# Performance work log

Measured on AMD Instinct MI355X. Metric: run time of the kernel, lower is better.

The kernel has to match this reference:

```python
import jax, jax.numpy as jnp
import numpy as np

B, S, DEC, ENC, ATTN = 64, 1024, 1024, 1024, 1024

def setup_inputs() -> dict:
    key = jax.random.key(0)
    k1, k2, k3, k4, k5 = jax.random.split(key, 5)
    hidden = jax.random.normal(k1, (B, DEC), dtype=jnp.float32)
    encoder_outputs = jax.random.normal(k2, (B, S, ENC), dtype=jnp.float32)
    # nn.Linear(dec+enc -> attn_dim): weight [attn, dec+enc], bias [attn]
    fan_in = DEC + ENC
    bound = 1.0 / np.sqrt(fan_in)
    W_attn = jax.random.uniform(k3, (ATTN, fan_in), dtype=jnp.float32, minval=-bound, maxval=bound)
    b_attn = jax.random.uniform(k4, (ATTN,), dtype=jnp.float32, minval=-bound, maxval=bound)
    # v = torch.rand(attn_dim) -> uniform [0,1)
    v = jax.random.uniform(k5, (ATTN,), dtype=jnp.float32)
    return {"hidden": hidden, "encoder_outputs": encoder_outputs,
            "W_attn": W_attn, "b_attn": b_attn, "v": v}

def reference(hidden, encoder_outputs, W_attn, b_attn, v):
    # hidden: [B, DEC], encoder_outputs: [B, S, ENC]
    b, s, _ = encoder_outputs.shape
    h = jnp.broadcast_to(hidden[:, None, :], (b, s, hidden.shape[-1]))
    combined = jnp.concatenate([h, encoder_outputs], axis=-1)        # [B, S, DEC+ENC]
    energy = jnp.tanh(jnp.einsum('bsf,af->bsa', combined, W_attn) + b_attn)  # [B, S, ATTN]
    scores = jnp.einsum('bsa,a->bs', energy, v)                      # [B, S]
    attn_weights = jax.nn.softmax(scores, axis=1)                    # [B, S]
    context = jnp.einsum('bs,bse->be', attn_weights, encoder_outputs)[:, None, :]  # [B, 1, ENC]
    return context
```

## Files before the change

kernel.cpp:

```cpp
#include <hip/hip_runtime.h>
#include <hip/hip_bf16.h>
#include <stdint.h>

#define NB 64
#define NS 1024
#define NE 1024
#define NA 1024
#define NF 2048
#define LDP 144

typedef __attribute__((ext_vector_type(8))) short   short8;
typedef __attribute__((ext_vector_type(4))) short   short4v;
typedef __attribute__((ext_vector_type(4))) float   f32x4;
typedef __attribute__((ext_vector_type(8))) __bf16  bf16x8;

__device__ __forceinline__ unsigned short f2bf(float x) {
  union { float f; unsigned u; } v; v.f = x;
  unsigned r = v.u + 0x7fffu + ((v.u >> 16) & 1u);
  return (unsigned short)(r >> 16);
}
__device__ __forceinline__ float bf2f(unsigned short h) {
  union { unsigned u; float f; } v; v.u = ((unsigned)h) << 16;
  return v.f;
}
__device__ __forceinline__ float tanh_fast(float x) {
  float e = __expf(2.0f * x);
  return 1.0f - __fdividef(2.0f, e + 1.0f);
}
__device__ __forceinline__ short8 pack8(float4 a, float4 b) {
  short8 h;
  h[0]=(short)f2bf(a.x); h[1]=(short)f2bf(a.y); h[2]=(short)f2bf(a.z); h[3]=(short)f2bf(a.w);
  h[4]=(short)f2bf(b.x); h[5]=(short)f2bf(b.y); h[6]=(short)f2bf(b.z); h[7]=(short)f2bf(b.w);
  return h;
}
__device__ __forceinline__ void gload_lds16(const void* g, void* l) {
  __builtin_amdgcn_global_load_lds((const __attribute__((address_space(1))) void*)g,
                                   (__attribute__((address_space(3))) void*)l, 16, 0, 0);
}

__global__ __launch_bounds__(256) void k_pre(const float* __restrict__ hidden,
                                             const float* __restrict__ W,
                                             const float* __restrict__ bias,
                                             float* __restrict__ u_,
                                             float4* __restrict__ scz,
                                             float4* __restrict__ outz,
                                             short8* __restrict__ Wb,
                                             const float4* __restrict__ encf,
                                             short8* __restrict__ encb) {
  const int bid = blockIdx.x;
  const int tid = threadIdx.x;
  if (bid < 512) {
    const int l = tid & 63;
    const int w = tid >> 6;
    const int a = (bid >> 1) * 4 + w;
    const int bh = bid & 1;
    const float* wrow = W + (size_t)a * NF;
    float4 wv[4];
    #pragma unroll
    for (int i = 0; i < 4; ++i) wv[i] = *(const float4*)(wrow + l * 4 + i * 256);
    const float ba = bias[a];
    for (int b = bh * 32; b < bh * 32 + 32; ++b) {
      const float* hrow = hidden + b * 1024;
      float s = 0.f;
      #pragma unroll
      for (int i = 0; i < 4; ++i) {
        float4 hv = *(const float4*)(hrow + l * 4 + i * 256);
        s += wv[i].x * hv.x + wv[i].y * hv.y + wv[i].z * hv.z + wv[i].w * hv.w;
      }
      #pragma unroll
      for (int m = 1; m < 64; m <<= 1) s += __shfl_xor(s, m);
      if (l == 0) u_[b * NA + a] = s + ba;
    }
  } else if (bid < 640) {
    const int i = (bid - 512) * 256 + tid;
    float4 z; z.x = z.y = z.z = z.w = 0.f;
    if (i < 16384) scz[i] = z;
    else           outz[i - 16384] = z;
  } else if (bid < 1152) {
    const int id = (bid - 640) * 256 + tid;
    const int a = id >> 7, ku = id & 127;
    const float* s = W + (size_t)a * NF + 1024 + ku * 8;
    Wb[id] = pack8(*(const float4*)s, *(const float4*)(s + 4));
  } else {
    const int n8 = NB * NS * NE / 8;
    int i = (bid - 1152) * 256 + tid;
    const int stride = 2048 * 256;
    for (; i < n8; i += stride) {
      float4 a = encf[2 * i], b = encf[2 * i + 1];
      encb[i] = pack8(a, b);
    }
  }
}

__global__ __launch_bounds__(256) void k_zero(float4* __restrict__ p, int n4) {
  int i = blockIdx.x * 256 + threadIdx.x;
  if (i < n4) { float4 z; z.x = z.y = z.z = z.w = 0.f; p[i] = z; }
}
__global__ __launch_bounds__(256) void k_conv_w(const float* __restrict__ W, short8* __restrict__ dst) {
  const int id = blockIdx.x * 256 + threadIdx.x;
  const int a = id >> 7, ku = id & 127;
  const float* s = W + (size_t)a * NF + 1024 + ku * 8;
  dst[id] = pack8(*(const float4*)s, *(const float4*)(s + 4));
}
__global__ __launch_bounds__(256) void k_u(const float* __restrict__ hidden,
                                           const float* __restrict__ W,
                                           const float* __restrict__ bias,
                                           float* __restrict__ u) {
  const int l = threadIdx.x & 63;
  const int w = threadIdx.x >> 6;
  const int a = (blockIdx.x >> 1) * 4 + w;
  const int bh = blockIdx.x & 1;
  const float* wrow = W + (size_t)a * NF;
  float4 wv[4];
  #pragma unroll
  for (int i = 0; i < 4; ++i) wv[i] = *(const float4*)(wrow + l * 4 + i * 256);
  const float ba = bias[a];
  for (int b = bh * 32; b < bh * 32 + 32; ++b) {
    const float* hrow = hidden + b * 1024;
    float s = 0.f;
    #pragma unroll
    for (int i = 0; i < 4; ++i) {
      float4 hv = *(const float4*)(hrow + l * 4 + i * 256);
      s += wv[i].x * hv.x + wv[i].y * hv.y + wv[i].z * hv.z + wv[i].w * hv.w;
    }
    #pragma unroll
    for (int m = 1; m < 64; m <<= 1) s += __shfl_xor(s, m);
    if (l == 0) u[b * NA + a] = s + ba;
  }
}

__global__ __launch_bounds__(512, 2) void k_main256(const unsigned short* __restrict__ Ab,
                                                    const unsigned short* __restrict__ Bb,
                                                    const float* __restrict__ u_,
                                                    const float* __restrict__ v_,
                                                    float* __restrict__ scores) {
  __shared__ __align__(16) char smem[2 * 65536];

  const int tid = threadIdx.x;
  const int l = tid & 63;
  const int w = tid >> 6;
  const int wr = w >> 2, wc = w & 3;
  const int d = blockIdx.x;
  const int xcd = d & 7, q = d >> 3;
  const int rt = xcd * 32 + (q >> 2);
  const int ct = q & 3;
  const int b = rt >> 2;
  const int lh = l >> 4, l15 = l & 15, l7 = l & 7;

  const int ssk = ((tid & 7) ^ ((tid >> 3) & 7)) * 8;
  const unsigned short* aS = Ab + (size_t)(rt * 256 + (tid >> 3)) * NE + ssk;
  const unsigned short* bS = Bb + (size_t)(ct * 256 + (tid >> 3)) * NE + ssk;
  const int wdst = w * 1024;

  f32x4 acc[8][4] = {};

#define STAGE256(tt) do { \
    char* dst_ = smem + (((tt) & 1) << 16); \
    const unsigned short* a_ = aS + (size_t)(tt) * 64; \
    const unsigned short* b_ = bS + (size_t)(tt) * 64; \
    gload_lds16(a_,                    dst_ + wdst); \
    gload_lds16(a_ + (size_t) 64 * NE, dst_ +  64 * 128 + wdst); \
    gload_lds16(a_ + (size_t)128 * NE, dst_ + 128 * 128 + wdst); \
    gload_lds16(a_ + (size_t)192 * NE, dst_ + 192 * 128 + wdst); \
    gload_lds16(b_,                    dst_ + 32768 + wdst); \
    gload_lds16(b_ + (size_t) 64 * NE, dst_ + 32768 +  64 * 128 + wdst); \
    gload_lds16(b_ + (size_t)128 * NE, dst_ + 32768 + 128 * 128 + wdst); \
    gload_lds16(b_ + (size_t)192 * NE, dst_ + 32768 + 192 * 128 + wdst); } while (0)

  STAGE256(0);

  for (int t = 0; t < 16; ++t) {
    asm volatile("s_waitcnt vmcnt(0)" ::: "memory");
    asm volatile("s_barrier" ::: "memory");
    if (t < 15) STAGE256(t + 1);

    const char* As = smem + ((t & 1) << 16);
    const char* Bs = As + 32768;

    bf16x8 areg[8][2];
    #pragma unroll
    for (int rf = 0; rf < 8; ++rf)
      #pragma unroll
      for (int kh = 0; kh < 2; ++kh)
        areg[rf][kh] = *(const bf16x8*)(As + (wr * 128 + rf * 16 + l15) * 128
                                           + (((kh * 4 + lh) ^ l7) << 4));
    #pragma unroll
    for (int cfh = 0; cfh < 2; ++cfh) {
      bf16x8 breg[2][2];
      #pragma unroll
      for (int c2 = 0; c2 < 2; ++c2)
        #pragma unroll
        for (int kh = 0; kh < 2; ++kh)
          breg[c2][kh] = *(const bf16x8*)(Bs + (wc * 64 + (cfh * 2 + c2) * 16 + l15) * 128
                                             + (((kh * 4 + lh) ^ l7) << 4));
      __builtin_amdgcn_s_setprio(1);
      #pragma unroll
      for (int rf = 0; rf < 8; ++rf)
        #pragma unroll
        for (int c2 = 0; c2 < 2; ++c2)
          #pragma unroll
          for (int kh = 0; kh < 2; ++kh)
            acc[rf][cfh * 2 + c2] = __builtin_amdgcn_mfma_f32_16x16x32_bf16(
                areg[rf][kh], breg[c2][kh], acc[rf][cfh * 2 + c2], 0, 0, 0);
      __builtin_amdgcn_s_setprio(0);
    }
  }
#undef STAGE256

  const int colb = ct * 256 + wc * 64 + l15;
  float uv[4], vv[4];
  #pragma unroll
  for (int cf = 0; cf < 4; ++cf) {
    const int c = colb + cf * 16;
    uv[cf] = u_[b * NA + c];
    vv[cf] = v_[c];
  }
  #pragma unroll
  for (int rf = 0; rf < 8; ++rf) {
    #pragma unroll
    for (int reg = 0; reg < 4; ++reg) {
      float sacc = 0.f;
      #pragma unroll
      for (int cf = 0; cf < 4; ++cf)
        sacc += tanh_fast(acc[rf][cf][reg] + uv[cf]) * vv[cf];
      sacc += __shfl_xor(sacc, 1);
      sacc += __shfl_xor(sacc, 2);
      sacc += __shfl_xor(sacc, 4);
      sacc += __shfl_xor(sacc, 8);
      if (l15 == 0) {
        const int m = rt * 256 + wr * 128 + rf * 16 + lh * 4 + reg;
        atomicAdd(&scores[m], sacc);
      }
    }
  }
}

__global__ __launch_bounds__(256) void k_smctx(const float* __restrict__ sc,
                                               const unsigned short* __restrict__ encb,
                                               float* __restrict__ out) {
  const int b = blockIdx.x >> 4, scn = blockIdx.x & 15;
  const int t = threadIdx.x;
  __shared__ float rmax[4], rsum[4];
  __shared__ float wbuf[NS];

  float4 x = *(const float4*)(sc + b * NS + t * 4);
  float mx = fmaxf(fmaxf(x.x, x.y), fmaxf(x.z, x.w));
  #pragma unroll
  for (int m = 1; m < 64; m <<= 1) mx = fmaxf(mx, __shfl_xor(mx, m));
  if ((t & 63) == 0) rmax[t >> 6] = mx;
  __syncthreads();
  mx = fmaxf(fmaxf(rmax[0], rmax[1]), fmaxf(rmax[2], rmax[3]));
  float e0 = __expf(x.x - mx), e1 = __expf(x.y - mx);
  float e2 = __expf(x.z - mx), e3 = __expf(x.w - mx);
  float sm = e0 + e1 + e2 + e3;
  #pragma unroll
  for (int m = 1; m < 64; m <<= 1) sm += __shfl_xor(sm, m);
  if ((t & 63) == 0) rsum[t >> 6] = sm;
  __syncthreads();
  sm = rsum[0] + rsum[1] + rsum[2] + rsum[3];
  const float inv = 1.0f / sm;
  wbuf[t * 4 + 0] = e0 * inv;
  wbuf[t * 4 + 1] = e1 * inv;
  wbuf[t * 4 + 2] = e2 * inv;
  wbuf[t * 4 + 3] = e3 * inv;
  __syncthreads();

  float a0 = 0.f, a1 = 0.f, a2 = 0.f, a3 = 0.f;
  for (int s = scn * 64; s < scn * 64 + 64; ++s) {
    const float wv = wbuf[s];
    const size_t base = ((size_t)(b * NS + s)) * NE + t * 4;
    short4v hv = *(const short4v*)(encb + base);
    a0 += wv * bf2f((unsigned short)hv[0]);
    a1 += wv * bf2f((unsigned short)hv[1]);
    a2 += wv * bf2f((unsigned short)hv[2]);
    a3 += wv * bf2f((unsigned short)hv[3]);
  }
  float* c = out + b * NE + t * 4;
  atomicAdd(c + 0, a0); atomicAdd(c + 1, a1);
  atomicAdd(c + 2, a2); atomicAdd(c + 3, a3);
}

template <int ACONV, int BCONV>
__global__ __launch_bounds__(256) void k_main_rs(const void* __restrict__ Asrc,
                                                 const void* __restrict__ Bsrc,
                                                 const float* __restrict__ u_,
                                                 const float* __restrict__ v_,
                                                 float* __restrict__ scores) {
  __shared__ __align__(16) char smemf[2 * 128 * LDP];
  char* As = smemf;
  char* Bs = smemf + 128 * LDP;
  const int tid = threadIdx.x;
  const int l = tid & 63;
  const int w = tid >> 6;
  const int wr = w >> 1, wc = w & 1;
  const int d = blockIdx.x;
  const int rt = (d & 7) * 64 + (d >> 6);
  const int ct = (d >> 3) & 7;
  const int b = rt >> 3;
  const int l7 = l & 7, lh = l >> 4, l15 = l & 15;
  const int srow = w * 8 + (l >> 3);
  f32x4 acc[4][4] = {};
  for (int kt = 0; kt < 16; ++kt) {
    const int k0 = kt * 64;
    __syncthreads();
    #pragma unroll
    for (int r = 0; r < 4; ++r) {
      const int row = r * 32 + srow;
      short8 val;
      if constexpr (ACONV) {
        const float* s = (const float*)Asrc + (size_t)(rt * 128 + row) * NE + k0 + l7 * 8;
        val = pack8(*(const float4*)s, *(const float4*)(s + 4));
      } else {
        val = *(const short8*)((const unsigned short*)Asrc + (size_t)(rt * 128 + row) * NE + k0 + l7 * 8);
      }
      *(short8*)(As + row * LDP + l7 * 16) = val;
    }
    #pragma unroll
    for (int r = 0; r < 4; ++r) {
      const int row = r * 32 + srow;
      short8 val;
      if constexpr (BCONV) {
        const float* s = (const float*)Bsrc + (size_t)(ct * 128 + row) * NF + 1024 + k0 + l7 * 8;
        val = pack8(*(const float4*)s, *(const float4*)(s + 4));
      } else {
        val = *(const short8*)((const unsigned short*)Bsrc + (size_t)(ct * 128 + row) * NE + k0 + l7 * 8);
      }
      *(short8*)(Bs + row * LDP + l7 * 16) = val;
    }
    __syncthreads();
    #pragma unroll
    for (int ks = 0; ks < 2; ++ks) {
      bf16x8 af[4], bfr[4];
      const int ku = (ks * 4 + lh) * 16;
      #pragma unroll
      for (int f = 0; f < 4; ++f) {
        af[f]  = *(const bf16x8*)(As + (wr * 64 + f * 16 + l15) * LDP + ku);
        bfr[f] = *(const bf16x8*)(Bs + (wc * 64 + f * 16 + l15) * LDP + ku);
      }
      #pragma unroll
      for (int i = 0; i < 4; ++i)
        #pragma unroll
        for (int jj = 0; jj < 4; ++jj)
          acc[i][jj] = __builtin_amdgcn_mfma_f32_16x16x32_bf16(af[i], bfr[jj], acc[i][jj], 0, 0, 0);
    }
  }
  const int colb = ct * 128 + wc * 64 + l15;
  float uv[4], vv[4];
  #pragma unroll
  for (int jj = 0; jj < 4; ++jj) {
    const int c = colb + jj * 16;
    uv[jj] = u_[b * NA + c];
    vv[jj] = v_[c];
  }
  #pragma unroll
  for (int i = 0; i < 4; ++i) {
    #pragma unroll
    for (int reg = 0; reg < 4; ++reg) {
      float sacc = 0.f;
      #pragma unroll
      for (int jj = 0; jj < 4; ++jj)
        sacc += tanh_fast(acc[i][jj][reg] + uv[jj]) * vv[jj];
      sacc += __shfl_xor(sacc, 1);
      sacc += __shfl_xor(sacc, 2);
      sacc += __shfl_xor(sacc, 4);
      sacc += __shfl_xor(sacc, 8);
      if (l15 == 0) {
        const int m = rt * 128 + wr * 64 + i * 16 + lh * 4 + reg;
        atomicAdd(&scores[m], sacc);
      }
    }
  }
}

__global__ __launch_bounds__(256) void k_softmax(float* __restrict__ sc) {
  const int b = blockIdx.x, t = threadIdx.x;
  float4 x = *(float4*)(sc + b * NS + t * 4);
  float mx = fmaxf(fmaxf(x.x, x.y), fmaxf(x.z, x.w));
  #pragma unroll
  for (int m = 1; m < 64; m <<= 1) mx = fmaxf(mx, __shfl_xor(mx, m));
  __shared__ float rmax[4], rsum[4];
  if ((t & 63) == 0) rmax[t >> 6] = mx;
  __syncthreads();
  mx = fmaxf(fmaxf(rmax[0], rmax[1]), fmaxf(rmax[2], rmax[3]));
  float e0 = __expf(x.x - mx), e1 = __expf(x.y - mx);
  float e2 = __expf(x.z - mx), e3 = __expf(x.w - mx);
  float sm = e0 + e1 + e2 + e3;
  #pragma unroll
  for (int m = 1; m < 64; m <<= 1) sm += __shfl_xor(sm, m);
  if ((t & 63) == 0) rsum[t >> 6] = sm;
  __syncthreads();
  sm = rsum[0] + rsum[1] + rsum[2] + rsum[3];
  const float inv = 1.0f / sm;
  float4 o; o.x = e0 * inv; o.y = e1 * inv; o.z = e2 * inv; o.w = e3 * inv;
  *(float4*)(sc + b * NS + t * 4) = o;
}
template <int CONV>
__global__ __launch_bounds__(256) void k_ctx(const void* __restrict__ encsrc,
                                             const float* __restrict__ wgt,
                                             float* __restrict__ ctx) {
  const int b = blockIdx.x >> 4, scn = blockIdx.x & 15;
  const int t = threadIdx.x;
  float a0 = 0.f, a1 = 0.f, a2 = 0.f, a3 = 0.f;
  for (int s = scn * 64; s < scn * 64 + 64; ++s) {
    const float wv = wgt[b * NS + s];
    const size_t base = ((size_t)(b * NS + s)) * NE + t * 4;
    if constexpr (CONV) {
      float4 x = *((const float4*)((const float*)encsrc + base));
      a0 += wv * x.x; a1 += wv * x.y; a2 += wv * x.z; a3 += wv * x.w;
    } else {
      short4v hv = *(const short4v*)((const unsigned short*)encsrc + base);
      a0 += wv * bf2f((unsigned short)hv[0]);
      a1 += wv * bf2f((unsigned short)hv[1]);
      a2 += wv * bf2f((unsigned short)hv[2]);
      a3 += wv * bf2f((unsigned short)hv[3]);
    }
  }
  float* c = ctx + b * NE + t * 4;
  atomicAdd(c + 0, a0); atomicAdd(c + 1, a1);
  atomicAdd(c + 2, a2); atomicAdd(c + 3, a3);
}
__global__ __launch_bounds__(256) void k_out(const float* __restrict__ ctx,
                                             float* __restrict__ out) {
  const int i = blockIdx.x * 256 + threadIdx.x;
  float4 x = *(const float4*)(ctx + i * 4);
  *(float4*)(out + i * 4) = x;
}

extern "C" void kernel_launch(void* const* d_in, const int* in_sizes, int n_in,
                              void* d_out, int out_size, void* d_ws, size_t ws_size,
                              hipStream_t stream) {
  const float* hidden = (const float*)d_in[0];
  const float* enc    = (const float*)d_in[1];
  const float* W      = (const float*)d_in[2];
  const float* bias   = (const float*)d_in[3];
  const float* v      = (const float*)d_in[4];
  (void)in_sizes; (void)n_in; (void)out_size;

  char* ws = (char*)d_ws;
  const size_t T0 = (4ull << 20) + (128ull << 20);
  const size_t T1 = (3ull << 20);
  const int tier = (ws_size >= T0) ? 0 : ((ws_size >= T1) ? 1 : 2);

  unsigned short* Wb   = (unsigned short*)ws;
  unsigned short* encb = (unsigned short*)(ws + (4ull << 20));
  float* u_  = (tier < 2) ? (float*)(ws + (2ull << 20)) : (float*)ws;
  float* sc  = u_ + NB * NA;
  float* ctx = sc + NB * NS;

  if (tier == 0) {
    k_pre<<<3200, 256, 0, stream>>>(hidden, W, bias, u_, (float4*)sc, (float4*)d_out,
                                    (short8*)Wb, (const float4*)enc, (short8*)encb);
    k_main256<<<1024, 512, 0, stream>>>(encb, Wb, u_, v, sc);
    k_smctx<<<1024, 256, 0, stream>>>(sc, encb, (float*)d_out);
  } else if (tier == 1) {
    k_u<<<512, 256, 0, stream>>>(hidden, W, bias, u_);
    k_zero<<<128, 256, 0, stream>>>((float4*)sc, (NB * NS + NB * NE) / 4);
    k_conv_w<<<512, 256, 0, stream>>>(W, (short8*)Wb);
    k_main_rs<1, 0><<<4096, 256, 0, stream>>>(enc, Wb, u_, v, sc);
    k_softmax<<<64, 256, 0, stream>>>(sc);
    k_ctx<1><<<1024, 256, 0, stream>>>(enc, sc, ctx);
    k_out<<<64, 256, 0, stream>>>(ctx, (float*)d_out);
  } else {
    k_u<<<512, 256, 0, stream>>>(hidden, W, bias, u_);
    k_zero<<<128, 256, 0, stream>>>((float4*)sc, (NB * NS + NB * NE) / 4);
    k_main_rs<1, 1><<<4096, 256, 0, stream>>>(enc, W, u_, v, sc);
    k_softmax<<<64, 256, 0, stream>>>(sc);
    k_ctx<1><<<1024, 256, 0, stream>>>(enc, sc, ctx);
    k_out<<<64, 256, 0, stream>>>(ctx, (float*)d_out);
  }
}
```

Before: 251.1 us.

## Replace 256x256 GEMM tile with 128x128 tile and 4-wave blocks

The main bf16 MFMA kernel moves from 256x256 output tiles with 8 waves and 128KB of LDS to 128x128 tiles with 4 waves and 64KB of LDS. It launches 4096 blocks instead of 1024 and uses a new block-to-tile mapping across XCDs. The aim is more resident blocks per CU and better load balance. The cost is lower arithmetic intensity per tile, roughly doubling global/L2 traffic for the A and B operands, and more atomic adds into the scores buffer.

```diff
diff --git a/kernel.cpp b/kernel.cpp
--- a/kernel.cpp
+++ b/kernel.cpp
@@ -129,106 +129,95 @@
   }
 }
 
-__global__ __launch_bounds__(512, 2) void k_main256(const unsigned short* __restrict__ Ab,
-                                                    const unsigned short* __restrict__ Bb,
-                                                    const float* __restrict__ u_,
-                                                    const float* __restrict__ v_,
-                                                    float* __restrict__ scores) {
-  __shared__ __align__(16) char smem[2 * 65536];
+__global__ __launch_bounds__(256, 2) void k_main128d(const unsigned short* __restrict__ Ab,
+                                                     const unsigned short* __restrict__ Bb,
+                                                     const float* __restrict__ u_,
+                                                     const float* __restrict__ v_,
+                                                     float* __restrict__ scores) {
+  __shared__ __align__(16) char smem[2 * 32768];
 
   const int tid = threadIdx.x;
   const int l = tid & 63;
   const int w = tid >> 6;
-  const int wr = w >> 2, wc = w & 3;
+  const int wr = w >> 1, wc = w & 1;
   const int d = blockIdx.x;
-  const int xcd = d & 7, q = d >> 3;
-  const int rt = xcd * 32 + (q >> 2);
-  const int ct = q & 3;
-  const int b = rt >> 2;
-  const int lh = l >> 4, l15 = l & 15, l7 = l & 7;
-
-  const int ssk = ((tid & 7) ^ ((tid >> 3) & 7)) * 8;
-  const unsigned short* aS = Ab + (size_t)(rt * 256 + (tid >> 3)) * NE + ssk;
-  const unsigned short* bS = Bb + (size_t)(ct * 256 + (tid >> 3)) * NE + ssk;
-  const int wdst = w * 1024;
-
-  f32x4 acc[8][4] = {};
-
-#define STAGE256(tt) do { \
-    char* dst_ = smem + (((tt) & 1) << 16); \
+  const int rt = (d & 7) * 64 + (d >> 6);
+  const int ct = (d >> 3) & 7;
+  const int b = rt >> 3;
+  const int l7 = l & 7, lh = l >> 4, l15 = l & 15;
+  const int srow = w * 32 + (l >> 3);
+  const int sk   = (l7 ^ (l >> 3)) * 8;
+
+  const unsigned short* aS = Ab + (size_t)(rt * 128 + srow) * NE + sk;
+  const unsigned short* bS = Bb + (size_t)(ct * 128 + srow) * NE + sk;
+
+  f32x4 acc[4][4] = {};
+
+#define STG128(tt) do { \
+    char* dst_ = smem + (((tt) & 1) << 15); \
     const unsigned short* a_ = aS + (size_t)(tt) * 64; \
     const unsigned short* b_ = bS + (size_t)(tt) * 64; \
-    gload_lds16(a_,                    dst_ + wdst); \
-    gload_lds16(a_ + (size_t) 64 * NE, dst_ +  64 * 128 + wdst); \
-    gload_lds16(a_ + (size_t)128 * NE, dst_ + 128 * 128 + wdst); \
-    gload_lds16(a_ + (size_t)192 * NE, dst_ + 192 * 128 + wdst); \
-    gload_lds16(b_,                    dst_ + 32768 + wdst); \
-    gload_lds16(b_ + (size_t) 64 * NE, dst_ + 32768 +  64 * 128 + wdst); \
-    gload_lds16(b_ + (size_t)128 * NE, dst_ + 32768 + 128 * 128 + wdst); \
-    gload_lds16(b_ + (size_t)192 * NE, dst_ + 32768 + 192 * 128 + wdst); } while (0)
-
-  STAGE256(0);
+    gload_lds16(a_,                   dst_ + (w * 32 +  0) * 128); \
+    gload_lds16(a_ + (size_t) 8 * NE, dst_ + (w * 32 +  8) * 128); \
+    gload_lds16(a_ + (size_t)16 * NE, dst_ + (w * 32 + 16) * 128); \
+    gload_lds16(a_ + (size_t)24 * NE, dst_ + (w * 32 + 24) * 128); \
+    gload_lds16(b_,                   dst_ + 16384 + (w * 32 +  0) * 128); \
+    gload_lds16(b_ + (size_t) 8 * NE, dst_ + 16384 + (w * 32 +  8) * 128); \
+    gload_lds16(b_ + (size_t)16 * NE, dst_ + 16384 + (w * 32 + 16) * 128); \
+    gload_lds16(b_ + (size_t)24 * NE, dst_ + 16384 + (w * 32 + 24) * 128); } while (0)
+
+  STG128(0);
 
   for (int t = 0; t < 16; ++t) {
     asm volatile("s_waitcnt vmcnt(0)" ::: "memory");
     asm volatile("s_barrier" ::: "memory");
-    if (t < 15) STAGE256(t + 1);
-
-    const char* As = smem + ((t & 1) << 16);
-    const char* Bs = As + 32768;
-
-    bf16x8 areg[8][2];
-    #pragma unroll
-    for (int rf = 0; rf < 8; ++rf)
-      #pragma unroll
-      for (int kh = 0; kh < 2; ++kh)
-        areg[rf][kh] = *(const bf16x8*)(As + (wr * 128 + rf * 16 + l15) * 128
-                                           + (((kh * 4 + lh) ^ l7) << 4));
-    #pragma unroll
-    for (int cfh = 0; cfh < 2; ++cfh) {
-      bf16x8 breg[2][2];
-      #pragma unroll
-      for (int c2 = 0; c2 < 2; ++c2)
+    if (t < 15) STG128(t + 1);
+
+    const char* As = smem + ((t & 1) << 15);
+    const char* Bs = As + 16384;
+
+    #pragma unroll
+    for (int ks = 0; ks < 2; ++ks) {
+      bf16x8 af[4], bfr[4];
+      const int ku = ((ks * 4 + lh) ^ l7) * 16;
+      #pragma unroll
+      for (int f = 0; f < 4; ++f) {
+        af[f]  = *(const bf16x8*)(As + (wr * 64 + f * 16 + l15) * 128 + ku);
+        bfr[f] = *(const bf16x8*)(Bs + (wc * 64 + f * 16 + l15) * 128 + ku);
+      }
+      __builtin_amdgcn_s_setprio(1);
+      #pragma unroll
+      for (int i = 0; i < 4; ++i)
         #pragma unroll
-        for (int kh = 0; kh < 2; ++kh)
-          breg[c2][kh] = *(const bf16x8*)(Bs + (wc * 64 + (cfh * 2 + c2) * 16 + l15) * 128
-                                             + (((kh * 4 + lh) ^ l7) << 4));
-      __builtin_amdgcn_s_setprio(1);
-      #pragma unroll
-      for (int rf = 0; rf < 8; ++rf)
-        #pragma unroll
-        for (int c2 = 0; c2 < 2; ++c2)
-          #pragma unroll
-          for (int kh = 0; kh < 2; ++kh)
-            acc[rf][cfh * 2 + c2] = __builtin_amdgcn_mfma_f32_16x16x32_bf16(
-                areg[rf][kh], breg[c2][kh], acc[rf][cfh * 2 + c2], 0, 0, 0);
+        for (int jj = 0; jj < 4; ++jj)
+          acc[i][jj] = __builtin_amdgcn_mfma_f32_16x16x32_bf16(af[i], bfr[jj], acc[i][jj], 0, 0, 0);
       __builtin_amdgcn_s_setprio(0);
     }
   }
-#undef STAGE256
-
-  const int colb = ct * 256 + wc * 64 + l15;
+#undef STG128
+
+  const int colb = ct * 128 + wc * 64 + l15;
   float uv[4], vv[4];
   #pragma unroll
-  for (int cf = 0; cf < 4; ++cf) {
-    const int c = colb + cf * 16;
-    uv[cf] = u_[b * NA + c];
-    vv[cf] = v_[c];
-  }
-  #pragma unroll
-  for (int rf = 0; rf < 8; ++rf) {
+  for (int jj = 0; jj < 4; ++jj) {
+    const int c = colb + jj * 16;
+    uv[jj] = u_[b * NA + c];
+    vv[jj] = v_[c];
+  }
+  #pragma unroll
+  for (int i = 0; i < 4; ++i) {
     #pragma unroll
     for (int reg = 0; reg < 4; ++reg) {
       float sacc = 0.f;
       #pragma unroll
-      for (int cf = 0; cf < 4; ++cf)
-        sacc += tanh_fast(acc[rf][cf][reg] + uv[cf]) * vv[cf];
+      for (int jj = 0; jj < 4; ++jj)
+        sacc += tanh_fast(acc[i][jj][reg] + uv[jj]) * vv[jj];
       sacc += __shfl_xor(sacc, 1);
       sacc += __shfl_xor(sacc, 2);
       sacc += __shfl_xor(sacc, 4);
       sacc += __shfl_xor(sacc, 8);
       if (l15 == 0) {
-        const int m = rt * 256 + wr * 128 + rf * 16 + lh * 4 + reg;
+        const int m = rt * 128 + wr * 64 + i * 16 + lh * 4 + reg;
         atomicAdd(&scores[m], sacc);
       }
     }
@@ -450,7 +439,7 @@
   if (tier == 0) {
     k_pre<<<3200, 256, 0, stream>>>(hidden, W, bias, u_, (float4*)sc, (float4*)d_out,
                                     (short8*)Wb, (const float4*)enc, (short8*)encb);
-    k_main256<<<1024, 512, 0, stream>>>(encb, Wb, u_, v, sc);
+    k_main128d<<<4096, 256, 0, stream>>>(encb, Wb, u_, v, sc);
     k_smctx<<<1024, 256, 0, stream>>>(sc, encb, (float*)d_out);
   } else if (tier == 1) {
     k_u<<<512, 256, 0, stream>>>(hidden, W, bias, u_);
```

New measurement: 299.7 us. 1.19x slower.
